# Performance work log

Measured on AMD Instinct MI355X. Metric: run time of the kernel, lower is better.

Reference implementation:

```python
import jax, jax.numpy as jnp
import numpy as np

EMBED = 1536
HEADS = 12
EPS = 1e-5


def _layernorm(x, gamma, beta):
    mu = x.mean(axis=-1, keepdims=True)
    var = ((x - mu) ** 2).mean(axis=-1, keepdims=True)
    return (x - mu) * jax.lax.rsqrt(var + EPS) * gamma + beta


def setup_inputs() -> dict:
    key = jax.random.key(0)
    ks = jax.random.split(key, 8)
    N, L, E = 8, 2048, EMBED
    x = jax.random.normal(ks[0], (N, L, E), dtype=jnp.float32)
    s = 0.02
    Wv = jax.random.normal(ks[1], (E, E), dtype=jnp.float32) * s
    Wk = jax.random.normal(ks[2], (E, E), dtype=jnp.float32) * s
    Wq = jax.random.normal(ks[3], (E, E), dtype=jnp.float32) * s
    Wo = jax.random.normal(ks[4], (E, E), dtype=jnp.float32) * s
    bo = jnp.zeros((E,), dtype=jnp.float32)
    gamma = jnp.ones((E,), dtype=jnp.float32)
    beta = jnp.zeros((E,), dtype=jnp.float32)
    return {"combined_embeddings": x, "Wv": Wv, "Wk": Wk, "Wq": Wq,
            "Wo": Wo, "bo": bo, "gamma": gamma, "beta": beta}


def reference(combined_embeddings, Wv, Wk, Wq, Wo, bo, gamma, beta):
    x = combined_embeddings
    N, L, E = x.shape
    H, hd = HEADS, E // HEADS
    # projections (torch Linear: x @ W^T), reshape to (N, H, L, hd)
    v = (x @ Wv.T).reshape(N, L, H, hd).transpose(0, 2, 1, 3)
    k = (x @ Wk.T).reshape(N, L, H, hd).transpose(0, 2, 1, 3)
    q = (x @ Wq.T).reshape(N, L, H, hd).transpose(0, 2, 1, 3)
    # NOTE: faithful to the source, einsum labels treat axis1 (heads) as q/k
    # and axis2 (sequence) as h -> heads-over-heads attention per position.
    energy = jnp.einsum('nqhd,nkhd->nhqk', q, k)  # (N, L, H, H)
    attention = jax.nn.softmax(energy / jnp.sqrt(jnp.float32(E)), axis=3)
    out = jnp.einsum('nhql,nlhd->nqhd', attention, v)  # (N, H, L, hd)
    out = out.transpose(0, 2, 1, 3).reshape(N, L, E)
    out = out @ Wo.T + bo
    out = _layernorm(out + x, gamma, beta)
    # small extra attention
    e_actions = out[:, 2:][None]          # (1, N, L-2, E)
    e_state = out.mean(axis=1)[None]      # (1, N, E)
    scores = jnp.matmul(e_state, jnp.swapaxes(e_actions, -2, -1))
    scores = scores / jnp.sqrt(jnp.float32(E))   # (1, N, N, L-2)
    weights = jax.nn.softmax(scores, axis=-1)
    attended = jnp.matmul(weights, e_actions)    # (1, N, N, E)
    return attended, weights
```

## Files before the change

kernel.cpp:

```cpp
#include <hip/hip_runtime.h>
#include <stdint.h>

typedef unsigned short u16;
typedef __bf16 bf16_t;
typedef bf16_t bf16x8 __attribute__((ext_vector_type(8)));
typedef float f32x4 __attribute__((ext_vector_type(4)));

#define E_DIM 1536
#define N_B 8
#define L_SEQ 2048
#define NT 2046
#define SCALE 0.025515518f
#define LN_EPS 1e-5f
#define NTILES 24

__device__ __forceinline__ u16 f2b(float f) {
  union { float f; uint32_t u; } v; v.f = f;
  uint32_t u = v.u + 0x7FFFu + ((v.u >> 16) & 1u);
  return (u16)(u >> 16);
}
__device__ __forceinline__ float b2f(u16 h) {
  union { uint32_t u; float f; } v; v.u = ((uint32_t)h) << 16; return v.f;
}

__device__ __forceinline__ void gload16(const u16* g, const bf16_t* l) {
  __builtin_amdgcn_global_load_lds((const __attribute__((address_space(1))) void*)g,
                                   (__attribute__((address_space(3))) void*)l,
                                   16, 0, 0);
}

#define BAR()   __builtin_amdgcn_s_barrier()
#define LGKM0() asm volatile("s_waitcnt lgkmcnt(0)" ::: "memory")
#define VM4()   asm volatile("s_waitcnt vmcnt(4)" ::: "memory")
#define VM0()   asm volatile("s_waitcnt vmcnt(0)" ::: "memory")

__global__ void cvt_kernel(const float* __restrict__ in, u16* __restrict__ out, int nvec) {
  int i = blockIdx.x * 256 + threadIdx.x;
  if (i < nvec) {
    float4 f = ((const float4*)in)[i];
    ushort4 u;
    u.x = f2b(f.x); u.y = f2b(f.y); u.z = f2b(f.z); u.w = f2b(f.w);
    ((ushort4*)out)[i] = u;
  }
}

template<int FUSED>
__launch_bounds__(512, 2)
__global__ void gemm8(const u16* __restrict__ Ag,
                      const u16* __restrict__ B0w, const u16* __restrict__ B1w,
                      const u16* __restrict__ B2w,
                      u16* __restrict__ C0, u16* __restrict__ C1, u16* __restrict__ C2,
                      float* __restrict__ Cf, const float* __restrict__ bias,
                      const float* __restrict__ resid)
{
  extern __shared__ __attribute__((aligned(16))) bf16_t lds[];

  const int flat = (blockIdx.z * gridDim.y + blockIdx.y) * gridDim.x + blockIdx.x;
  const int xcd = flat & 7, bb_ = flat >> 3;
  const int gl = bb_ / 24, jj = bb_ % 24;
  const int g = gl * 8 + xcd;
  const int zz = g >> 4;
  const int gy = g & 15;
  const int tx = jj >> 2;
  const int ty = gy * 4 + (jj & 3);
  const int rowA = ty * 256, colB = tx * 256;

  const u16* Bg; u16* Cb;
  if (zz == 0)      { Bg = B0w; Cb = C0; }
  else if (zz == 1) { Bg = B1w; Cb = C1; }
  else              { Bg = B2w; Cb = C2; }

  const int tid = threadIdx.x;
  const int w = tid >> 6, lane = tid & 63;
  const int wr = w >> 2, wc = w & 3;

  const int rl = lane & 15, lsl = lane >> 4;
  const int sw8 = (lsl ^ ((rl >> 1) & 3)) * 8;
  const int arow = (wr * 128 + rl) * 32 + sw8;
  const int brow = (wc * 64 + rl) * 32 + sw8;

  const int r0s = tid >> 2, sps = tid & 3;
  const int sws = (sps ^ ((r0s >> 1) & 3)) * 8;
  const size_t sA0 = (size_t)(rowA + r0s) * E_DIM + sws;
  const size_t sA1 = (size_t)(rowA + 128 + r0s) * E_DIM + sws;
  const size_t sB0 = (size_t)(colB + r0s) * E_DIM + sws;
  const size_t sB1 = (size_t)(colB + 128 + r0s) * E_DIM + sws;
  const int wb0 = w * 512, wb1 = 4096 + w * 512;

  f32x4 acc[8][4];
#pragma unroll
  for (int m = 0; m < 8; ++m)
#pragma unroll
    for (int n = 0; n < 4; ++n)
#pragma unroll
      for (int q = 0; q < 4; ++q) acc[m][n][q] = 0.0f;

  gload16(Ag + sA0,      lds + 0     + wb0);  gload16(Ag + sA1,      lds + 0     + wb1);
  gload16(Bg + sB0,      lds + 32768 + wb0);  gload16(Bg + sB1,      lds + 32768 + wb1);
  gload16(Ag + sA0 + 32, lds + 8192  + wb0);  gload16(Ag + sA1 + 32, lds + 8192  + wb1);
  gload16(Bg + sB0 + 32, lds + 40960 + wb0);  gload16(Bg + sB1 + 32, lds + 40960 + wb1);
  gload16(Bg + sB0 + 64, lds + 49152 + wb0);  gload16(Bg + sB1 + 64, lds + 49152 + wb1);
  gload16(Ag + sA0 + 64, lds + 16384 + wb0);  gload16(Ag + sA1 + 64, lds + 16384 + wb1);
  VM4();
  BAR();

#pragma unroll 2
  for (int t = 0; t < NTILES; ++t) {
    const int cur = t & 1, nxt = cur ^ 1;
    const int Ak0 = (cur * 2 + 0) * 8192, Ak1 = (cur * 2 + 1) * 8192;
    const int Bk0 = 32768 + (cur * 2 + 0) * 8192, Bk1 = 32768 + (cur * 2 + 1) * 8192;
    const int AkN = (nxt * 2 + 1) * 8192, BkN = 32768 + (nxt * 2 + 1) * 8192;
    const int AkC = Ak0, BkC = Bk0;
    bf16x8 af[4], bfr[4];

#pragma unroll
    for (int i = 0; i < 4; ++i) af[i] = *(const bf16x8*)&lds[Ak0 + arow + i * 512];
#pragma unroll
    for (int n = 0; n < 4; ++n) bfr[n] = *(const bf16x8*)&lds[Bk0 + brow + n * 512];
    if (t + 1 < NTILES) {
      gload16(Bg + sB0 + (t + 1) * 64 + 32, lds + BkN + wb0);
      gload16(Bg + sB1 + (t + 1) * 64 + 32, lds + BkN + wb1);
    }
    BAR(); LGKM0();
    __builtin_amdgcn_s_setprio(1);
#pragma unroll
    for (int i = 0; i < 4; ++i)
#pragma unroll
      for (int n = 0; n < 4; ++n)
        acc[i][n] = __builtin_amdgcn_mfma_f32_16x16x32_bf16(af[i], bfr[n], acc[i][n], 0, 0, 0);
    __builtin_amdgcn_s_setprio(0);
    BAR();

#pragma unroll
    for (int i = 0; i < 4; ++i) af[i] = *(const bf16x8*)&lds[Ak0 + arow + (4 + i) * 512];
    if (t + 1 < NTILES) {
      gload16(Ag + sA0 + (t + 1) * 64 + 32, lds + AkN + wb0);
      gload16(Ag + sA1 + (t + 1) * 64 + 32, lds + AkN + wb1);
    }
    BAR(); LGKM0();
    __builtin_amdgcn_s_setprio(1);
#pragma unroll
    for (int i = 0; i < 4; ++i)
#pragma unroll
      for (int n = 0; n < 4; ++n)
        acc[4 + i][n] = __builtin_amdgcn_mfma_f32_16x16x32_bf16(af[i], bfr[n], acc[4 + i][n], 0, 0, 0);
    __builtin_amdgcn_s_setprio(0);
    BAR();

#pragma unroll
    for (int i = 0; i < 4; ++i) af[i] = *(const bf16x8*)&lds[Ak1 + arow + i * 512];
#pragma unroll
    for (int n = 0; n < 4; ++n) bfr[n] = *(const bf16x8*)&lds[Bk1 + brow + n * 512];
    if (t + 2 < NTILES) {
      gload16(Bg + sB0 + (t + 2) * 64, lds + BkC + wb0);
      gload16(Bg + sB1 + (t + 2) * 64, lds + BkC + wb1);
    }
    BAR(); LGKM0();
    __builtin_amdgcn_s_setprio(1);
#pragma unroll
    for (int i = 0; i < 4; ++i)
#pragma unroll
      for (int n = 0; n < 4; ++n)
        acc[i][n] = __builtin_amdgcn_mfma_f32_16x16x32_bf16(af[i], bfr[n], acc[i][n], 0, 0, 0);
    __builtin_amdgcn_s_setprio(0);
    BAR();

#pragma unroll
    for (int i = 0; i < 4; ++i) af[i] = *(const bf16x8*)&lds[Ak1 + arow + (4 + i) * 512];
    if (t + 2 < NTILES) {
      gload16(Ag + sA0 + (t + 2) * 64, lds + AkC + wb0);
      gload16(Ag + sA1 + (t + 2) * 64, lds + AkC + wb1);
    }
    BAR(); LGKM0();
    __builtin_amdgcn_s_setprio(1);
#pragma unroll
    for (int i = 0; i < 4; ++i)
#pragma unroll
      for (int n = 0; n < 4; ++n)
        acc[4 + i][n] = __builtin_amdgcn_mfma_f32_16x16x32_bf16(af[i], bfr[n], acc[4 + i][n], 0, 0, 0);
    __builtin_amdgcn_s_setprio(0);
    if (t < NTILES - 2) { VM4(); } else { VM0(); }
    BAR();
  }

  const int r0 = (lane >> 4) * 4;
#pragma unroll
  for (int m = 0; m < 8; ++m) {
#pragma unroll
    for (int n = 0; n < 4; ++n) {
      const int gcol = colB + wc * 64 + n * 16 + rl;
#pragma unroll
      for (int q = 0; q < 4; ++q) {
        const int grow = rowA + wr * 128 + m * 16 + r0 + q;
        const size_t idx = (size_t)grow * E_DIM + gcol;
        if (FUSED) Cf[idx] = acc[m][n][q] + bias[gcol] + resid[idx];
        else       Cb[idx] = f2b(acc[m][n][q]);
      }
    }
  }
}

__launch_bounds__(256)
__global__ void headmix(const u16* __restrict__ qb, const u16* __restrict__ kb,
                        const u16* __restrict__ vb, u16* __restrict__ aob)
{
  __shared__ float qs[12 * 132], ks2[12 * 132], vs[12 * 132];
  __shared__ float att[12][12];
  const int tid = threadIdx.x;
  const size_t base = (size_t)blockIdx.x * E_DIM;

  for (int e = tid; e < E_DIM; e += 256) {
    int i = e >> 7, d = e & 127, p = i * 132 + d;
    qs[p]  = b2f(qb[base + e]);
    ks2[p] = b2f(kb[base + e]);
    vs[p]  = b2f(vb[base + e]);
  }
  __syncthreads();

  if (tid < 144) {
    int i = tid / 12, j = tid % 12;
    float s = 0.f;
#pragma unroll 8
    for (int d = 0; d < 128; ++d) s += qs[i * 132 + d] * ks2[j * 132 + d];
    att[i][j] = s * SCALE;
  }
  __syncthreads();

  if (tid < 12) {
    float mx = att[tid][0];
#pragma unroll
    for (int j = 1; j < 12; ++j) mx = fmaxf(mx, att[tid][j]);
    float ev[12], sum = 0.f;
#pragma unroll
    for (int j = 0; j < 12; ++j) { ev[j] = expf(att[tid][j] - mx); sum += ev[j]; }
    float inv = 1.f / sum;
#pragma unroll
    for (int j = 0; j < 12; ++j) att[tid][j] = ev[j] * inv;
  }
  __syncthreads();

  for (int e = tid; e < E_DIM; e += 256) {
    int i = e >> 7, d = e & 127;
    float o = 0.f;
#pragma unroll
    for (int j = 0; j < 12; ++j) o += att[i][j] * vs[j * 132 + d];
    aob[base + e] = f2b(o);
  }
}

__launch_bounds__(256)
__global__ void ln_kernel(float* __restrict__ p, const float* __restrict__ gamma,
                          const float* __restrict__ beta)
{
  __shared__ float rs[4], rq[4];
  __shared__ float mean_s, rstd_s;
  const int tid = threadIdx.x, w = tid >> 6, lane = tid & 63;
  float* row = p + (size_t)blockIdx.x * E_DIM;

  float v[6], s = 0.f, sq = 0.f;
#pragma unroll
  for (int i = 0; i < 6; ++i) {
    v[i] = row[tid + i * 256];
    s += v[i]; sq += v[i] * v[i];
  }
#pragma unroll
  for (int off = 32; off > 0; off >>= 1) {
    s  += __shfl_down(s, off);
    sq += __shfl_down(sq, off);
  }
  if (lane == 0) { rs[w] = s; rq[w] = sq; }
  __syncthreads();
  if (tid == 0) {
    float S = rs[0] + rs[1] + rs[2] + rs[3];
    float Q = rq[0] + rq[1] + rq[2] + rq[3];
    float mu = S * (1.f / 1536.f);
    float var = Q * (1.f / 1536.f) - mu * mu;
    mean_s = mu; rstd_s = rsqrtf(var + LN_EPS);
  }
  __syncthreads();
  const float mu = mean_s, rstd = rstd_s;
#pragma unroll
  for (int i = 0; i < 6; ++i) {
    int e = tid + i * 256;
    row[e] = (v[i] - mu) * rstd * gamma[e] + beta[e];
  }
}

__global__ void estate_partial(const float* __restrict__ outp, float* __restrict__ part)
{
  const int e = blockIdx.x * 256 + threadIdx.x;
  const int b = blockIdx.y, z = blockIdx.z;
  const float* p = outp + ((size_t)b * L_SEQ + z * 256) * E_DIM + e;
  float acc = 0.f;
  for (int l = 0; l < 256; ++l) acc += p[(size_t)l * E_DIM];
  part[(size_t)(z * N_B + b) * E_DIM + e] = acc;
}
__global__ void estate_reduce(const float* __restrict__ part, float* __restrict__ est)
{
  const int i = blockIdx.x * 256 + threadIdx.x;
  if (i < N_B * E_DIM) {
    float s = 0.f;
#pragma unroll
    for (int z = 0; z < 8; ++z) s += part[(size_t)z * N_B * E_DIM + i];
    est[i] = s * (1.f / 2048.f);
  }
}

__launch_bounds__(256)
__global__ void scores_kernel(const float* __restrict__ outp, const float* __restrict__ est,
                              float* __restrict__ wout)
{
  __shared__ float es[N_B * E_DIM];
  const int tid = threadIdx.x, wv = tid >> 6, lane = tid & 63;
  const int b = blockIdx.y;
  for (int i = tid; i < N_B * E_DIM; i += 256) es[i] = est[i];
  __syncthreads();

  for (int ti = 0; ti < 16; ++ti) {
    int t = blockIdx.x * 64 + wv * 16 + ti;
    if (t >= NT) continue;
    const float* row = outp + ((size_t)b * L_SEQ + 2 + t) * E_DIM;
    float a[8];
#pragma unroll
    for (int s = 0; s < 8; ++s) a[s] = 0.f;
    for (int c = 0; c < 24; ++c) {
      int idx = c * 64 + lane;
      float val = row[idx];
#pragma unroll
      for (int s = 0; s < 8; ++s) a[s] += es[s * E_DIM + idx] * val;
    }
#pragma unroll
    for (int off = 32; off > 0; off >>= 1)
#pragma unroll
      for (int s = 0; s < 8; ++s) a[s] += __shfl_down(a[s], off);
    if (lane == 0) {
#pragma unroll
      for (int s = 0; s < 8; ++s)
        wout[(size_t)(b * N_B + s) * NT + t] = a[s] * SCALE;
    }
  }
}

__launch_bounds__(256)
__global__ void softmax_w(float* __restrict__ wbase)
{
  float* p = wbase + (size_t)blockIdx.x * NT;
  __shared__ float r1[4], r2[4];
  __shared__ float bmax, bsum;
  const int tid = threadIdx.x, wv = tid >> 6, lane = tid & 63;

  float vals[8], mx = -1e30f;
#pragma unroll
  for (int i = 0; i < 8; ++i) {
    int t = tid + i * 256;
    vals[i] = (t < NT) ? p[t] : -1e30f;
    mx = fmaxf(mx, vals[i]);
  }
#pragma unroll
  for (int off = 32; off > 0; off >>= 1) mx = fmaxf(mx, __shfl_down(mx, off));
  if (lane == 0) r1[wv] = mx;
  __syncthreads();
  if (tid == 0) bmax = fmaxf(fmaxf(r1[0], r1[1]), fmaxf(r1[2], r1[3]));
  __syncthreads();
  mx = bmax;

  float sum = 0.f;
#pragma unroll
  for (int i = 0; i < 8; ++i) {
    int t = tid + i * 256;
    if (t < NT) { vals[i] = expf(vals[i] - mx); sum += vals[i]; }
  }
#pragma unroll
  for (int off = 32; off > 0; off >>= 1) sum += __shfl_down(sum, off);
  if (lane == 0) r2[wv] = sum;
  __syncthreads();
  if (tid == 0) bsum = r2[0] + r2[1] + r2[2] + r2[3];
  __syncthreads();
  const float inv = 1.f / bsum;
#pragma unroll
  for (int i = 0; i < 8; ++i) {
    int t = tid + i * 256;
    if (t < NT) p[t] = vals[i] * inv;
  }
}

__launch_bounds__(256)
__global__ void attended_partial(const float* __restrict__ outp, const float* __restrict__ wts,
                                 float* __restrict__ part)
{
  const int tid = threadIdx.x;
  const int e = blockIdx.x * 256 + tid;
  const int b = blockIdx.y, z = blockIdx.z;
  __shared__ float wl[8][256];
  float a[8];
#pragma unroll
  for (int s = 0; s < 8; ++s) a[s] = 0.f;

  const int tbeg = z * 512;
  const int tend = (tbeg + 512 < NT) ? tbeg + 512 : NT;
  for (int tb = tbeg; tb < tend; tb += 256) {
    const int cnt = (tend - tb < 256) ? (tend - tb) : 256;
    __syncthreads();
    for (int i = tid; i < 8 * 256; i += 256) {
      int s = i >> 8, tt = i & 255;
      wl[s][tt] = (tt < cnt) ? wts[(size_t)(b * N_B + s) * NT + tb + tt] : 0.f;
    }
    __syncthreads();
    for (int tt = 0; tt < cnt; ++tt) {
      float val = outp[((size_t)b * L_SEQ + 2 + tb + tt) * E_DIM + e];
#pragma unroll
      for (int s = 0; s < 8; ++s) a[s] += wl[s][tt] * val;
    }
  }
#pragma unroll
  for (int s = 0; s < 8; ++s)
    part[(((size_t)z * N_B + b) * N_B + s) * E_DIM + e] = a[s];
}
__global__ void attended_reduce(const float* __restrict__ part, float* __restrict__ outp)
{
  const int i = blockIdx.x * 256 + threadIdx.x;
  float s = 0.f;
#pragma unroll
  for (int z = 0; z < 4; ++z) s += part[(size_t)z * N_B * N_B * E_DIM + i];
  outp[i] = s;
}

extern "C" void kernel_launch(void* const* d_in, const int* in_sizes, int n_in,
                              void* d_out, int out_size, void* d_ws, size_t ws_size,
                              hipStream_t stream)
{
  (void)in_sizes; (void)n_in; (void)out_size; (void)ws_size;
  const float* x     = (const float*)d_in[0];
  const float* Wv    = (const float*)d_in[1];
  const float* Wk    = (const float*)d_in[2];
  const float* Wq    = (const float*)d_in[3];
  const float* Wo    = (const float*)d_in[4];
  const float* bo    = (const float*)d_in[5];
  const float* gamma = (const float*)d_in[6];
  const float* beta  = (const float*)d_in[7];
  float* out = (float*)d_out;

  char* ws = (char*)d_ws;
  size_t off = 0;
  auto alloc = [&](size_t bytes) -> void* {
    void* p = ws + off;
    off += (bytes + 255) & ~(size_t)255;
    return p;
  };
  const size_t ME = (size_t)16384 * E_DIM;
  const size_t WE = (size_t)E_DIM * E_DIM;
  u16*   xb    = (u16*)alloc(ME * 2);
  u16*   wqb   = (u16*)alloc(WE * 2);
  u16*   wkb   = (u16*)alloc(WE * 2);
  u16*   wvb   = (u16*)alloc(WE * 2);
  u16*   wob   = (u16*)alloc(WE * 2);
  u16*   qb    = (u16*)alloc(ME * 2);
  u16*   kb    = (u16*)alloc(ME * 2);
  u16*   vb    = (u16*)alloc(ME * 2);
  u16*   aob   = (u16*)alloc(ME * 2);
  float* lnbuf = (float*)alloc(ME * 4);
  float* est   = (float*)alloc((size_t)N_B * E_DIM * 4);
  float* estp  = (float*)alloc((size_t)8 * N_B * E_DIM * 4);
  float* attp  = (float*)alloc((size_t)4 * N_B * N_B * E_DIM * 4);

  float* wout = out + 98304;

  hipFuncSetAttribute(reinterpret_cast<const void*>(gemm8<0>),
                      hipFuncAttributeMaxDynamicSharedMemorySize, 131072);
  hipFuncSetAttribute(reinterpret_cast<const void*>(gemm8<1>),
                      hipFuncAttributeMaxDynamicSharedMemorySize, 131072);

  cvt_kernel<<<dim3((6291456 + 255) / 256), 256, 0, stream>>>(x, xb, 6291456);
  cvt_kernel<<<dim3((589824 + 255) / 256), 256, 0, stream>>>(Wq, wqb, 589824);
  cvt_kernel<<<dim3((589824 + 255) / 256), 256, 0, stream>>>(Wk, wkb, 589824);
  cvt_kernel<<<dim3((589824 + 255) / 256), 256, 0, stream>>>(Wv, wvb, 589824);
  cvt_kernel<<<dim3((589824 + 255) / 256), 256, 0, stream>>>(Wo, wob, 589824);

  gemm8<0><<<dim3(6, 64, 3), 512, 131072, stream>>>(
      xb, wqb, wkb, wvb, qb, kb, vb, nullptr, nullptr, nullptr);

  headmix<<<dim3(16384), 256, 0, stream>>>(qb, kb, vb, aob);

  gemm8<1><<<dim3(6, 64, 1), 512, 131072, stream>>>(
      aob, wob, wob, wob, nullptr, nullptr, nullptr, lnbuf, bo, x);

  ln_kernel<<<dim3(16384), 256, 0, stream>>>(lnbuf, gamma, beta);

  estate_partial<<<dim3(6, 8, 8), 256, 0, stream>>>(lnbuf, estp);
  estate_reduce<<<dim3(48), 256, 0, stream>>>(estp, est);

  scores_kernel<<<dim3(32, 8), 256, 0, stream>>>(lnbuf, est, wout);
  softmax_w<<<dim3(64), 256, 0, stream>>>(wout);

  attended_partial<<<dim3(6, 8, 4), 256, 0, stream>>>(lnbuf, wout, attp);
  attended_reduce<<<dim3(384), 256, 0, stream>>>(attp, out);
}
```

Baseline: 576.9 us.

## Restructure GEMM main loop into two-phase register-prefetched pipeline with fewer barriers

The GEMM inner loop moves from four sub-phases, each with its own barrier and lgkmcnt wait, to two phases per iteration. Each phase runs a full 8x4 MFMA block while the next k-slice's A/B fragments are read from LDS into a second register set, and sched_barrier fences stop the compiler from reordering across the phases. This is meant to hide LDS read latency behind MFMA work and halve the barrier count. The cost is doubled fragment registers (a0/a1/b0/b1), which may hurt occupancy under the 512x2 launch bounds. Removing the explicit lgkmcnt waits also leaves ordering to the compiler.

```diff
diff --git a/kernel.cpp b/kernel.cpp
--- a/kernel.cpp
+++ b/kernel.cpp
@@ -30,7 +30,7 @@
 }
 
 #define BAR()   __builtin_amdgcn_s_barrier()
-#define LGKM0() asm volatile("s_waitcnt lgkmcnt(0)" ::: "memory")
+#define SCHB()  __builtin_amdgcn_sched_barrier(0)
 #define VM4()   asm volatile("s_waitcnt vmcnt(4)" ::: "memory")
 #define VM0()   asm volatile("s_waitcnt vmcnt(0)" ::: "memory")
 
@@ -46,12 +46,12 @@
 
 template<int FUSED>
 __launch_bounds__(512, 2)
-__global__ void gemm8(const u16* __restrict__ Ag,
-                      const u16* __restrict__ B0w, const u16* __restrict__ B1w,
-                      const u16* __restrict__ B2w,
-                      u16* __restrict__ C0, u16* __restrict__ C1, u16* __restrict__ C2,
-                      float* __restrict__ Cf, const float* __restrict__ bias,
-                      const float* __restrict__ resid)
+__global__ void gemm2c(const u16* __restrict__ Ag,
+                       const u16* __restrict__ B0w, const u16* __restrict__ B1w,
+                       const u16* __restrict__ B2w,
+                       u16* __restrict__ C0, u16* __restrict__ C1, u16* __restrict__ C2,
+                       float* __restrict__ Cf, const float* __restrict__ bias,
+                       const float* __restrict__ resid)
 {
   extern __shared__ __attribute__((aligned(16))) bf16_t lds[];
 
@@ -99,87 +99,68 @@
   gload16(Bg + sB0,      lds + 32768 + wb0);  gload16(Bg + sB1,      lds + 32768 + wb1);
   gload16(Ag + sA0 + 32, lds + 8192  + wb0);  gload16(Ag + sA1 + 32, lds + 8192  + wb1);
   gload16(Bg + sB0 + 32, lds + 40960 + wb0);  gload16(Bg + sB1 + 32, lds + 40960 + wb1);
+  gload16(Ag + sA0 + 64, lds + 16384 + wb0);  gload16(Ag + sA1 + 64, lds + 16384 + wb1);
   gload16(Bg + sB0 + 64, lds + 49152 + wb0);  gload16(Bg + sB1 + 64, lds + 49152 + wb1);
-  gload16(Ag + sA0 + 64, lds + 16384 + wb0);  gload16(Ag + sA1 + 64, lds + 16384 + wb1);
   VM4();
   BAR();
 
-#pragma unroll 2
+  bf16x8 a0[8], b0[4], a1[8], b1[4];
+#pragma unroll
+  for (int m = 0; m < 8; ++m) a0[m] = *(const bf16x8*)&lds[0 + arow + m * 512];
+#pragma unroll
+  for (int n = 0; n < 4; ++n) b0[n] = *(const bf16x8*)&lds[32768 + brow + n * 512];
+
   for (int t = 0; t < NTILES; ++t) {
     const int cur = t & 1, nxt = cur ^ 1;
-    const int Ak0 = (cur * 2 + 0) * 8192, Ak1 = (cur * 2 + 1) * 8192;
-    const int Bk0 = 32768 + (cur * 2 + 0) * 8192, Bk1 = 32768 + (cur * 2 + 1) * 8192;
-    const int AkN = (nxt * 2 + 1) * 8192, BkN = 32768 + (nxt * 2 + 1) * 8192;
-    const int AkC = Ak0, BkC = Bk0;
-    bf16x8 af[4], bfr[4];
-
-#pragma unroll
-    for (int i = 0; i < 4; ++i) af[i] = *(const bf16x8*)&lds[Ak0 + arow + i * 512];
-#pragma unroll
-    for (int n = 0; n < 4; ++n) bfr[n] = *(const bf16x8*)&lds[Bk0 + brow + n * 512];
+    const int Ak1 = (cur * 2 + 1) * 8192, Bk1 = 32768 + (cur * 2 + 1) * 8192;
+    const int AkN0 = nxt * 2 * 8192,      BkN0 = 32768 + nxt * 2 * 8192;
+    const int AkN1 = (nxt * 2 + 1) * 8192, BkN1 = 32768 + (nxt * 2 + 1) * 8192;
+
+#pragma unroll
+    for (int m = 0; m < 8; ++m) a1[m] = *(const bf16x8*)&lds[Ak1 + arow + m * 512];
+#pragma unroll
+    for (int n = 0; n < 4; ++n) b1[n] = *(const bf16x8*)&lds[Bk1 + brow + n * 512];
     if (t + 1 < NTILES) {
-      gload16(Bg + sB0 + (t + 1) * 64 + 32, lds + BkN + wb0);
-      gload16(Bg + sB1 + (t + 1) * 64 + 32, lds + BkN + wb1);
-    }
-    BAR(); LGKM0();
+      const size_t ko = (size_t)(t + 1) * 64 + 32;
+      gload16(Ag + sA0 + ko, lds + AkN1 + wb0);  gload16(Ag + sA1 + ko, lds + AkN1 + wb1);
+      gload16(Bg + sB0 + ko, lds + BkN1 + wb0);  gload16(Bg + sB1 + ko, lds + BkN1 + wb1);
+    }
+    SCHB();
     __builtin_amdgcn_s_setprio(1);
 #pragma unroll
-    for (int i = 0; i < 4; ++i)
+    for (int m = 0; m < 8; ++m)
 #pragma unroll
       for (int n = 0; n < 4; ++n)
-        acc[i][n] = __builtin_amdgcn_mfma_f32_16x16x32_bf16(af[i], bfr[n], acc[i][n], 0, 0, 0);
+        acc[m][n] = __builtin_amdgcn_mfma_f32_16x16x32_bf16(a0[m], b0[n], acc[m][n], 0, 0, 0);
     __builtin_amdgcn_s_setprio(0);
+    SCHB();
+    if (t + 1 < NTILES) { VM4(); }
     BAR();
 
-#pragma unroll
-    for (int i = 0; i < 4; ++i) af[i] = *(const bf16x8*)&lds[Ak0 + arow + (4 + i) * 512];
+    if (t + 2 < NTILES) {
+      const size_t ko = (size_t)(t + 2) * 64;
+      gload16(Ag + sA0 + ko, lds + cur * 2 * 8192 + wb0);
+      gload16(Ag + sA1 + ko, lds + cur * 2 * 8192 + wb1);
+      gload16(Bg + sB0 + ko, lds + 32768 + cur * 2 * 8192 + wb0);
+      gload16(Bg + sB1 + ko, lds + 32768 + cur * 2 * 8192 + wb1);
+    }
     if (t + 1 < NTILES) {
-      gload16(Ag + sA0 + (t + 1) * 64 + 32, lds + AkN + wb0);
-      gload16(Ag + sA1 + (t + 1) * 64 + 32, lds + AkN + wb1);
-    }
-    BAR(); LGKM0();
+#pragma unroll
+      for (int m = 0; m < 8; ++m) a0[m] = *(const bf16x8*)&lds[AkN0 + arow + m * 512];
+#pragma unroll
+      for (int n = 0; n < 4; ++n) b0[n] = *(const bf16x8*)&lds[BkN0 + brow + n * 512];
+    }
+    SCHB();
     __builtin_amdgcn_s_setprio(1);
 #pragma unroll
-    for (int i = 0; i < 4; ++i)
+    for (int m = 0; m < 8; ++m)
 #pragma unroll
       for (int n = 0; n < 4; ++n)
-        acc[4 + i][n] = __builtin_amdgcn_mfma_f32_16x16x32_bf16(af[i], bfr[n], acc[4 + i][n], 0, 0, 0);
+        acc[m][n] = __builtin_amdgcn_mfma_f32_16x16x32_bf16(a1[m], b1[n], acc[m][n], 0, 0, 0);
     __builtin_amdgcn_s_setprio(0);
-    BAR();
-
-#pragma unroll
-    for (int i = 0; i < 4; ++i) af[i] = *(const bf16x8*)&lds[Ak1 + arow + i * 512];
-#pragma unroll
-    for (int n = 0; n < 4; ++n) bfr[n] = *(const bf16x8*)&lds[Bk1 + brow + n * 512];
-    if (t + 2 < NTILES) {
-      gload16(Bg + sB0 + (t + 2) * 64, lds + BkC + wb0);
-      gload16(Bg + sB1 + (t + 2) * 64, lds + BkC + wb1);
-    }
-    BAR(); LGKM0();
-    __builtin_amdgcn_s_setprio(1);
-#pragma unroll
-    for (int i = 0; i < 4; ++i)
-#pragma unroll
-      for (int n = 0; n < 4; ++n)
-        acc[i][n] = __builtin_amdgcn_mfma_f32_16x16x32_bf16(af[i], bfr[n], acc[i][n], 0, 0, 0);
-    __builtin_amdgcn_s_setprio(0);
-    BAR();
-
-#pragma unroll
-    for (int i = 0; i < 4; ++i) af[i] = *(const bf16x8*)&lds[Ak1 + arow + (4 + i) * 512];
-    if (t + 2 < NTILES) {
-      gload16(Ag + sA0 + (t + 2) * 64, lds + AkC + wb0);
-      gload16(Ag + sA1 + (t + 2) * 64, lds + AkC + wb1);
-    }
-    BAR(); LGKM0();
-    __builtin_amdgcn_s_setprio(1);
-#pragma unroll
-    for (int i = 0; i < 4; ++i)
-#pragma unroll
-      for (int n = 0; n < 4; ++n)
-        acc[4 + i][n] = __builtin_amdgcn_mfma_f32_16x16x32_bf16(af[i], bfr[n], acc[4 + i][n], 0, 0, 0);
-    __builtin_amdgcn_s_setprio(0);
-    if (t < NTILES - 2) { VM4(); } else { VM0(); }
+    SCHB();
+    if (t + 2 < NTILES)      { VM4(); }
+    else if (t + 1 < NTILES) { VM0(); }
     BAR();
   }
 
@@ -465,9 +446,9 @@
 
   float* wout = out + 98304;
 
-  hipFuncSetAttribute(reinterpret_cast<const void*>(gemm8<0>),
+  hipFuncSetAttribute(reinterpret_cast<const void*>(gemm2c<0>),
                       hipFuncAttributeMaxDynamicSharedMemorySize, 131072);
-  hipFuncSetAttribute(reinterpret_cast<const void*>(gemm8<1>),
+  hipFuncSetAttribute(reinterpret_cast<const void*>(gemm2c<1>),
                       hipFuncAttributeMaxDynamicSharedMemorySize, 131072);
 
   cvt_kernel<<<dim3((6291456 + 255) / 256), 256, 0, stream>>>(x, xb, 6291456);
@@ -476,12 +457,12 @@
   cvt_kernel<<<dim3((589824 + 255) / 256), 256, 0, stream>>>(Wv, wvb, 589824);
   cvt_kernel<<<dim3((589824 + 255) / 256), 256, 0, stream>>>(Wo, wob, 589824);
 
-  gemm8<0><<<dim3(6, 64, 3), 512, 131072, stream>>>(
+  gemm2c<0><<<dim3(6, 64, 3), 512, 131072, stream>>>(
       xb, wqb, wkb, wvb, qb, kb, vb, nullptr, nullptr, nullptr);
 
   headmix<<<dim3(16384), 256, 0, stream>>>(qb, kb, vb, aob);
 
-  gemm8<1><<<dim3(6, 64, 1), 512, 131072, stream>>>(
+  gemm2c<1><<<dim3(6, 64, 1), 512, 131072, stream>>>(
       aob, wob, wob, wob, nullptr, nullptr, nullptr, lnbuf, bo, x);
 
   ln_kernel<<<dim3(16384), 256, 0, stream>>>(lnbuf, gamma, beta);
```

New measurement: 567.8 us. Within noise of the previous version (-1.6%).

## Convert GEMM LDS staging to a four-slot ring with deeper prefetch

Applied to the files above, without the earlier changes.

Replaces the double-buffered K-half scheme in the bf16 GEMM with a four-slot ring buffer for A and B. Three K-slices are prefetched up front, and each iteration issues loads two slices ahead, waiting with vmcnt(8) instead of vmcnt(4). The goal is to keep more global-to-LDS loads in flight so memory latency is better hidden behind MFMA work. It adds a wait point mid-iteration and makes the vmcnt accounting more fragile.

```diff
diff --git a/kernel.cpp b/kernel.cpp
--- a/kernel.cpp
+++ b/kernel.cpp
@@ -31,6 +31,7 @@
 
 #define BAR()   __builtin_amdgcn_s_barrier()
 #define LGKM0() asm volatile("s_waitcnt lgkmcnt(0)" ::: "memory")
+#define VM8()   asm volatile("s_waitcnt vmcnt(8)" ::: "memory")
 #define VM4()   asm volatile("s_waitcnt vmcnt(4)" ::: "memory")
 #define VM0()   asm volatile("s_waitcnt vmcnt(0)" ::: "memory")
 
@@ -46,7 +47,7 @@
 
 template<int FUSED>
 __launch_bounds__(512, 2)
-__global__ void gemm8(const u16* __restrict__ Ag,
+__global__ void gemmr(const u16* __restrict__ Ag,
                       const u16* __restrict__ B0w, const u16* __restrict__ B1w,
                       const u16* __restrict__ B2w,
                       u16* __restrict__ C0, u16* __restrict__ C1, u16* __restrict__ C2,
@@ -87,6 +88,19 @@
   const size_t sB1 = (size_t)(colB + 128 + r0s) * E_DIM + sws;
   const int wb0 = w * 512, wb1 = 4096 + w * 512;
 
+  auto stageA = [&](int u) {
+    const size_t ko = (size_t)u * 32;
+    bf16_t* d = lds + (u & 3) * 8192;
+    gload16(Ag + sA0 + ko, d + wb0);
+    gload16(Ag + sA1 + ko, d + wb1);
+  };
+  auto stageB = [&](int u) {
+    const size_t ko = (size_t)u * 32;
+    bf16_t* d = lds + 32768 + (u & 3) * 8192;
+    gload16(Bg + sB0 + ko, d + wb0);
+    gload16(Bg + sB1 + ko, d + wb1);
+  };
+
   f32x4 acc[8][4];
 #pragma unroll
   for (int m = 0; m < 8; ++m)
@@ -95,32 +109,22 @@
 #pragma unroll
       for (int q = 0; q < 4; ++q) acc[m][n][q] = 0.0f;
 
-  gload16(Ag + sA0,      lds + 0     + wb0);  gload16(Ag + sA1,      lds + 0     + wb1);
-  gload16(Bg + sB0,      lds + 32768 + wb0);  gload16(Bg + sB1,      lds + 32768 + wb1);
-  gload16(Ag + sA0 + 32, lds + 8192  + wb0);  gload16(Ag + sA1 + 32, lds + 8192  + wb1);
-  gload16(Bg + sB0 + 32, lds + 40960 + wb0);  gload16(Bg + sB1 + 32, lds + 40960 + wb1);
-  gload16(Bg + sB0 + 64, lds + 49152 + wb0);  gload16(Bg + sB1 + 64, lds + 49152 + wb1);
-  gload16(Ag + sA0 + 64, lds + 16384 + wb0);  gload16(Ag + sA1 + 64, lds + 16384 + wb1);
-  VM4();
+  stageA(0); stageB(0); stageA(1); stageB(1); stageA(2); stageB(2);
+  VM8();
   BAR();
 
 #pragma unroll 2
   for (int t = 0; t < NTILES; ++t) {
-    const int cur = t & 1, nxt = cur ^ 1;
-    const int Ak0 = (cur * 2 + 0) * 8192, Ak1 = (cur * 2 + 1) * 8192;
-    const int Bk0 = 32768 + (cur * 2 + 0) * 8192, Bk1 = 32768 + (cur * 2 + 1) * 8192;
-    const int AkN = (nxt * 2 + 1) * 8192, BkN = 32768 + (nxt * 2 + 1) * 8192;
-    const int AkC = Ak0, BkC = Bk0;
+    const int s0 = (2 * t) & 3, s1 = s0 + 1;
+    const int A0r = s0 * 8192, B0r = 32768 + s0 * 8192;
+    const int A1r = s1 * 8192, B1r = 32768 + s1 * 8192;
     bf16x8 af[4], bfr[4];
 
 #pragma unroll
-    for (int i = 0; i < 4; ++i) af[i] = *(const bf16x8*)&lds[Ak0 + arow + i * 512];
-#pragma unroll
-    for (int n = 0; n < 4; ++n) bfr[n] = *(const bf16x8*)&lds[Bk0 + brow + n * 512];
-    if (t + 1 < NTILES) {
-      gload16(Bg + sB0 + (t + 1) * 64 + 32, lds + BkN + wb0);
-      gload16(Bg + sB1 + (t + 1) * 64 + 32, lds + BkN + wb1);
-    }
+    for (int i = 0; i < 4; ++i) af[i] = *(const bf16x8*)&lds[A0r + arow + i * 512];
+#pragma unroll
+    for (int n = 0; n < 4; ++n) bfr[n] = *(const bf16x8*)&lds[B0r + brow + n * 512];
+    if (t < 23) stageA(2 * t + 3);
     BAR(); LGKM0();
     __builtin_amdgcn_s_setprio(1);
 #pragma unroll
@@ -132,11 +136,8 @@
     BAR();
 
 #pragma unroll
-    for (int i = 0; i < 4; ++i) af[i] = *(const bf16x8*)&lds[Ak0 + arow + (4 + i) * 512];
-    if (t + 1 < NTILES) {
-      gload16(Ag + sA0 + (t + 1) * 64 + 32, lds + AkN + wb0);
-      gload16(Ag + sA1 + (t + 1) * 64 + 32, lds + AkN + wb1);
-    }
+    for (int i = 0; i < 4; ++i) af[i] = *(const bf16x8*)&lds[A0r + arow + (4 + i) * 512];
+    if (t < 23) stageB(2 * t + 3);
     BAR(); LGKM0();
     __builtin_amdgcn_s_setprio(1);
 #pragma unroll
@@ -145,16 +146,14 @@
       for (int n = 0; n < 4; ++n)
         acc[4 + i][n] = __builtin_amdgcn_mfma_f32_16x16x32_bf16(af[i], bfr[n], acc[4 + i][n], 0, 0, 0);
     __builtin_amdgcn_s_setprio(0);
+    if (t < 23) { VM8(); } else { VM0(); }
     BAR();
 
 #pragma unroll
-    for (int i = 0; i < 4; ++i) af[i] = *(const bf16x8*)&lds[Ak1 + arow + i * 512];
-#pragma unroll
-    for (int n = 0; n < 4; ++n) bfr[n] = *(const bf16x8*)&lds[Bk1 + brow + n * 512];
-    if (t + 2 < NTILES) {
-      gload16(Bg + sB0 + (t + 2) * 64, lds + BkC + wb0);
-      gload16(Bg + sB1 + (t + 2) * 64, lds + BkC + wb1);
-    }
+    for (int i = 0; i < 4; ++i) af[i] = *(const bf16x8*)&lds[A1r + arow + i * 512];
+#pragma unroll
+    for (int n = 0; n < 4; ++n) bfr[n] = *(const bf16x8*)&lds[B1r + brow + n * 512];
+    if (t < 22) stageA(2 * t + 4);
     BAR(); LGKM0();
     __builtin_amdgcn_s_setprio(1);
 #pragma unroll
@@ -166,11 +165,8 @@
     BAR();
 
 #pragma unroll
-    for (int i = 0; i < 4; ++i) af[i] = *(const bf16x8*)&lds[Ak1 + arow + (4 + i) * 512];
-    if (t + 2 < NTILES) {
-      gload16(Ag + sA0 + (t + 2) * 64, lds + AkC + wb0);
-      gload16(Ag + sA1 + (t + 2) * 64, lds + AkC + wb1);
-    }
+    for (int i = 0; i < 4; ++i) af[i] = *(const bf16x8*)&lds[A1r + arow + (4 + i) * 512];
+    if (t < 22) stageB(2 * t + 4);
     BAR(); LGKM0();
     __builtin_amdgcn_s_setprio(1);
 #pragma unroll
@@ -179,7 +175,7 @@
       for (int n = 0; n < 4; ++n)
         acc[4 + i][n] = __builtin_amdgcn_mfma_f32_16x16x32_bf16(af[i], bfr[n], acc[4 + i][n], 0, 0, 0);
     __builtin_amdgcn_s_setprio(0);
-    if (t < NTILES - 2) { VM4(); } else { VM0(); }
+    if (t < 22) { VM8(); } else if (t == 22) { VM4(); }
     BAR();
   }
 
@@ -465,9 +461,9 @@
 
   float* wout = out + 98304;
 
-  hipFuncSetAttribute(reinterpret_cast<const void*>(gemm8<0>),
+  hipFuncSetAttribute(reinterpret_cast<const void*>(gemmr<0>),
                       hipFuncAttributeMaxDynamicSharedMemorySize, 131072);
-  hipFuncSetAttribute(reinterpret_cast<const void*>(gemm8<1>),
+  hipFuncSetAttribute(reinterpret_cast<const void*>(gemmr<1>),
                       hipFuncAttributeMaxDynamicSharedMemorySize, 131072);
 
   cvt_kernel<<<dim3((6291456 + 255) / 256), 256, 0, stream>>>(x, xb, 6291456);
@@ -476,12 +472,12 @@
   cvt_kernel<<<dim3((589824 + 255) / 256), 256, 0, stream>>>(Wv, wvb, 589824);
   cvt_kernel<<<dim3((589824 + 255) / 256), 256, 0, stream>>>(Wo, wob, 589824);
 
-  gemm8<0><<<dim3(6, 64, 3), 512, 131072, stream>>>(
+  gemmr<0><<<dim3(6, 64, 3), 512, 131072, stream>>>(
       xb, wqb, wkb, wvb, qb, kb, vb, nullptr, nullptr, nullptr);
 
   headmix<<<dim3(16384), 256, 0, stream>>>(qb, kb, vb, aob);
 
-  gemm8<1><<<dim3(6, 64, 1), 512, 131072, stream>>>(
+  gemmr<1><<<dim3(6, 64, 1), 512, 131072, stream>>>(
       aob, wob, wob, wob, nullptr, nullptr, nullptr, lnbuf, bo, x);
 
   ln_kernel<<<dim3(16384), 256, 0, stream>>>(lnbuf, gamma, beta);
```

New measurement: 573.4 us. Within noise of the previous version (-0.6%).
